# Performance work log

Measured on AMD Instinct MI355X. Metric: run time of the kernel, lower is better.

## Reference

```python
import jax, jax.numpy as jnp
import numpy as np

DIM = 128
GRID = 8
RED = 16  # LCBAM channel-attention reduction
B, L = 16, 4096


def setup_inputs() -> dict:
    key = jax.random.key(0)
    ks = jax.random.split(key, 8)
    scale = 1.0 / (np.sqrt(DIM) * np.sqrt(GRID))
    return {
        "x": jax.random.normal(ks[0], (B, L, DIM), jnp.float32),
        "n1_g": jnp.ones((DIM,), jnp.float32),
        "n1_b": jnp.zeros((DIM,), jnp.float32),
        "fk1_c": jax.random.normal(ks[1], (2, DIM, DIM, GRID), jnp.float32) * scale,
        "fk1_b": jnp.zeros((DIM,), jnp.float32),
        "n2_g": jnp.ones((DIM,), jnp.float32),
        "n2_b": jnp.zeros((DIM,), jnp.float32),
        "fk2_c": jax.random.normal(ks[2], (2, DIM, DIM, GRID), jnp.float32) * scale,
        "fk2_b": jnp.zeros((DIM,), jnp.float32),
        "w1": jax.random.normal(ks[3], (DIM // RED, DIM), jnp.float32) * 0.05,  # channel-MLP reduce
        "w2": jax.random.normal(ks[4], (DIM, DIM // RED), jnp.float32) * 0.05,  # channel-MLP expand
        "conv_w": jax.random.normal(ks[5], (1, 2, 7, 7), jnp.float32) * 0.05,   # spatial-attn 7x7 conv
    }


def _layernorm(x, g, b, eps=1e-5):
    m = jnp.mean(x, axis=-1, keepdims=True)
    v = jnp.var(x, axis=-1, keepdims=True)
    return (x - m) * jax.lax.rsqrt(v + eps) * g + b


def _fkan(x, coeffs, bias):
    # x: (B,L,I); coeffs: (2,O,I,G)
    k = jnp.arange(1, GRID + 1, dtype=x.dtype)          # (G,)
    ang = x[..., None] * k                               # (B,L,I,G)
    y = jnp.einsum("blig,oig->blo", jnp.cos(ang), coeffs[0])
    y = y + jnp.einsum("blig,oig->blo", jnp.sin(ang), coeffs[1])
    return y + bias


def reference(x, n1_g, n1_b, fk1_c, fk1_b, n2_g, n2_b, fk2_c, fk2_b, w1, w2, conv_w):
    residual = x
    out = _fkan(_layernorm(x, n1_g, n1_b), fk1_c, fk1_b)
    out = jax.nn.relu(out)
    out = _fkan(_layernorm(out, n2_g, n2_b), fk2_c, fk2_b)
    b, l, c = out.shape
    x4 = out.reshape(b, c, 1, l)  # faithful to torch .view (raw reshape, not transpose)
    # LCBAM channel attention: avg+max pool -> shared MLP -> sigmoid
    avg = jnp.mean(x4, axis=(2, 3))   # (B,C)
    mx = jnp.max(x4, axis=(2, 3))     # (B,C)
    mlp = lambda v: jax.nn.relu(v @ w1.T) @ w2.T
    ca = jax.nn.sigmoid(mlp(avg) + mlp(mx))[:, :, None, None]
    x4 = x4 * ca
    # LCBAM spatial attention: channel mean/max -> 7x7 conv -> sigmoid
    s_in = jnp.concatenate([jnp.mean(x4, axis=1, keepdims=True),
                            jnp.max(x4, axis=1, keepdims=True)], axis=1)  # (B,2,1,L)
    sa = jax.lax.conv_general_dilated(s_in, conv_w, (1, 1), ((3, 3), (3, 3)))
    x4 = x4 * jax.nn.sigmoid(sa)
    out = x4.reshape(b, l, c)
    return residual + out
```

## Files before the change

kernel.cpp:

```cpp
#include <hip/hip_runtime.h>
#include <math.h>

typedef unsigned short ushort_t;
typedef unsigned int uint_t;
typedef _Float16 half_t;

#define DIMC 128
#define NB 16
#define NL 4096

using f32x4 = __attribute__((ext_vector_type(4))) float;
using bf16x8 = __attribute__((ext_vector_type(8))) short;
using half4 = __attribute__((ext_vector_type(4))) half_t;

__device__ __forceinline__ ushort_t bf16rne(float f) {
  uint_t b = __float_as_uint(f);
  b += 0x7fffu + ((b >> 16) & 1u);
  return (ushort_t)(b >> 16);
}

__device__ __forceinline__ uint_t pkbf(float lo, float hi) {
  union { __bf16 h[2]; uint_t u; } u;
  u.h[0] = (__bf16)lo;
  u.h[1] = (__bf16)hi;
  return u.u;
}

__device__ __forceinline__ float bf2f(ushort_t u) {
  return __uint_as_float(((uint_t)u) << 16);
}

__global__ __launch_bounds__(256) void prep_coef_k(const float* __restrict__ fk1,
                                                   const float* __restrict__ fk2,
                                                   ushort_t* __restrict__ coefT) {
  int idx = blockIdx.x * 256 + threadIdx.x;
  int layer = idx >> 15;
  int rem = idx & 32767;
  int ci = rem >> 11;
  int n = (rem >> 8) & 7;
  int s = (rem >> 6) & 3;
  int l = rem & 63;
  int o = n * 16 + (l & 15);
  int kbase = ci * 128 + s * 32 + (l >> 4) * 8;
  const float* src = layer ? fk2 : fk1;
  uint_t p[4];
#pragma unroll
  for (int jj = 0; jj < 4; ++jj) {
    int k0 = kbase + jj * 2;
    int t0 = k0 & 1, g0 = (k0 >> 1) & 7, i0 = k0 >> 4;
    int k1 = k0 + 1;
    int t1 = k1 & 1, g1 = (k1 >> 1) & 7, i1 = k1 >> 4;
    ushort_t a = bf16rne(src[((t0 * DIMC + o) * DIMC + i0) * 8 + g0]);
    ushort_t b = bf16rne(src[((t1 * DIMC + o) * DIMC + i1) * 8 + g1]);
    p[jj] = (uint_t)a | ((uint_t)b << 16);
  }
  uint4 w;
  w.x = p[0]; w.y = p[1]; w.z = p[2]; w.w = p[3];
  *(uint4*)&coefT[idx * 8] = w;
}

constexpr int SXH = 132;

__global__ __launch_bounds__(256, 3) void fkan_main_k(
    const float* __restrict__ x,
    const float* __restrict__ n1g, const float* __restrict__ n1b,
    const float* __restrict__ fk1b,
    const float* __restrict__ n2g, const float* __restrict__ n2b,
    const float* __restrict__ fk2b,
    const ushort_t* __restrict__ coefT,
    ushort_t* __restrict__ out2,
    float* __restrict__ chanSum, float* __restrict__ chanMax) {

  __shared__ half_t xln[128 * SXH];

  const int tid = threadIdx.x;
  const int bid = blockIdx.x;
  const int lane = tid & 63;
  const int wid = tid >> 6;
  const int rowBase = wid * 32;
  const size_t tileBase = (size_t)bid * 128 * DIMC;

  {
    const float4* src = (const float4*)(x + tileBase + (size_t)rowBase * DIMC);
#pragma unroll
    for (int j = 0; j < 16; ++j) {
      int idx = j * 64 + lane;
      float4 v = src[idx];
      half4 h;
      h.x = (half_t)v.x; h.y = (half_t)v.y; h.z = (half_t)v.z; h.w = (half_t)v.w;
      *(half4*)&xln[(rowBase + (idx >> 5)) * SXH + (idx & 31) * 4] = h;
    }
  }

  auto layernorm = [&](const float* gg, const float* bb) {
    float g0 = gg[lane], g1 = gg[lane + 64];
    float be0 = bb[lane], be1 = bb[lane + 64];
#pragma unroll
    for (int j = 0; j < 32; ++j) {
      int t = rowBase + j;
      float v0 = (float)xln[t * SXH + lane], v1 = (float)xln[t * SXH + 64 + lane];
      float s = v0 + v1, q = v0 * v0 + v1 * v1;
#pragma unroll
      for (int m = 1; m < 64; m <<= 1) {
        s += __shfl_xor(s, m, 64);
        q += __shfl_xor(q, m, 64);
      }
      float mean = s * (1.0f / DIMC);
      float var = q * (1.0f / DIMC) - mean * mean;
      float rr = rsqrtf(var + 1e-5f);
      xln[t * SXH + lane] = (half_t)((v0 - mean) * rr * g0 + be0);
      xln[t * SXH + 64 + lane] = (half_t)((v1 - mean) * rr * g1 + be1);
    }
  };

  layernorm(n1g, n1b);

  const int hi = lane >> 4;
  const int hb = hi & 1;
  const half_t* xfr = &xln[(rowBase + (lane & 15)) * SXH + (hi >> 1)];

  auto featfrag = [&](int ci, int s, int mm) -> bf16x8 {
    float a = (float)xfr[mm * 16 * SXH + ci * 8 + s * 2];
    float s1, c1, s5, c5;
    __sincosf(a, &s1, &c1);
    __sincosf(5.0f * a, &s5, &c5);
    float cs = hb ? c5 : c1;
    float ss = hb ? s5 : s1;
    uint_t p0 = pkbf(cs, ss);
    float cn, sn;
    cn = cs * c1 - ss * s1; sn = ss * c1 + cs * s1; cs = cn; ss = sn;
    uint_t p1 = pkbf(cs, ss);
    cn = cs * c1 - ss * s1; sn = ss * c1 + cs * s1; cs = cn; ss = sn;
    uint_t p2 = pkbf(cs, ss);
    cn = cs * c1 - ss * s1; sn = ss * c1 + cs * s1; cs = cn; ss = sn;
    uint_t p3 = pkbf(cs, ss);
    union { uint_t u[4]; bf16x8 v; } r;
    r.u[0] = p0; r.u[1] = p1; r.u[2] = p2; r.u[3] = p3;
    return r.v;
  };

  f32x4 acc[8][2];

  auto ldB = [&](const ushort_t* cbase, int ci, int s, bf16x8 (&bf)[8]) {
#pragma unroll
    for (int nn = 0; nn < 8; ++nn)
      bf[nn] = *(const bf16x8*)(cbase +
          (size_t)((((ci * 8 + nn) * 4 + s) << 6) + lane) * 8);
  };

  auto mfma16 = [&](bf16x8 a0, bf16x8 a1, bf16x8 (&bf)[8]) {
    __builtin_amdgcn_s_setprio(1);
#pragma unroll
    for (int nn = 0; nn < 8; ++nn) {
      acc[nn][0] = __builtin_amdgcn_mfma_f32_16x16x32_bf16(a0, bf[nn],
                                                           acc[nn][0], 0, 0, 0);
      acc[nn][1] = __builtin_amdgcn_mfma_f32_16x16x32_bf16(a1, bf[nn],
                                                           acc[nn][1], 0, 0, 0);
    }
    __builtin_amdgcn_s_setprio(0);
  };

  auto run_layer = [&](const ushort_t* cbase) {
#pragma unroll
    for (int nn = 0; nn < 8; ++nn)
#pragma unroll
      for (int mm = 0; mm < 2; ++mm) acc[nn][mm] = (f32x4)(0.f);
#pragma unroll 1
    for (int ci = 0; ci < 16; ++ci) {
#pragma unroll
      for (int s = 0; s < 4; ++s) {
        bf16x8 bf[8];
        ldB(cbase, ci, s, bf);
        bf16x8 a0 = featfrag(ci, s, 0);
        bf16x8 a1 = featfrag(ci, s, 1);
        mfma16(a0, a1, bf);
      }
    }
  };

  run_layer(coefT);

#pragma unroll
  for (int nn = 0; nn < 8; ++nn) {
    int o = nn * 16 + (lane & 15);
    float bia = fk1b[o];
#pragma unroll
    for (int mm = 0; mm < 2; ++mm) {
      int trow = rowBase + mm * 16 + (lane >> 4) * 4;
#pragma unroll
      for (int r = 0; r < 4; ++r)
        xln[(trow + r) * SXH + o] = (half_t)fmaxf(acc[nn][mm][r] + bia, 0.f);
    }
  }

  layernorm(n2g, n2b);

  run_layer(coefT + 262144);

  float ls = 0.f, lm = -INFINITY;
#pragma unroll
  for (int nn = 0; nn < 8; ++nn) {
    int o = nn * 16 + (lane & 15);
    float bia = fk2b[o];
#pragma unroll
    for (int mm = 0; mm < 2; ++mm) {
      int trow = rowBase + mm * 16 + (lane >> 4) * 4;
#pragma unroll
      for (int r = 0; r < 4; ++r) {
        float v = acc[nn][mm][r] + bia;
        out2[tileBase + (size_t)(trow + r) * DIMC + o] = bf16rne(v);
        ls += v;
        lm = fmaxf(lm, v);
      }
    }
  }
#pragma unroll
  for (int m = 1; m < 64; m <<= 1) {
    ls += __shfl_xor(ls, m, 64);
    lm = fmaxf(lm, __shfl_xor(lm, m, 64));
  }
  if (lane == 0) {
    chanSum[bid * 4 + wid] = ls;
    chanMax[bid * 4 + wid] = lm;
  }
}

__global__ __launch_bounds__(128) void tail_k(
    const float* __restrict__ x, const ushort_t* __restrict__ out2,
    const float* __restrict__ chanSum, const float* __restrict__ chanMax,
    const float* __restrict__ w1, const float* __restrict__ w2,
    const float* __restrict__ convw, float* __restrict__ dout) {
  int b = blockIdx.x >> 5;
  int t = blockIdx.x & 31;
  int c = threadIdx.x;
  __shared__ float avs[DIMC], mxs[DIMC], hh[16], cas[DIMC];
  __shared__ float sM[134], sX[134];

  avs[c] = chanSum[b * DIMC + c] * (1.0f / NL);
  mxs[c] = chanMax[b * DIMC + c];
  __syncthreads();
  if (c < 16) {
    const float* v = (c < 8) ? avs : mxs;
    float a = 0.f;
    for (int i = 0; i < DIMC; ++i) a += v[i] * w1[(c & 7) * DIMC + i];
    hh[c] = fmaxf(a, 0.f);
  }
  __syncthreads();
  {
    float z = 0.f;
#pragma unroll
    for (int r = 0; r < 8; ++r) z += (hh[r] + hh[8 + r]) * w2[c * 8 + r];
    cas[c] = 1.0f / (1.0f + expf(-z));
  }
  __syncthreads();

  const ushort_t* o2b = out2 + (size_t)b * NL * DIMC;
  float s = 0.f, m = -INFINITY;
#pragma unroll 4
  for (int c4 = 0; c4 < 128; ++c4) {
    float v = bf2f(o2b[(size_t)(c4 * 32 + t) * DIMC + c]) * cas[c4];
    s += v;
    m = fmaxf(m, v);
  }
  sM[c + 3] = s * (1.0f / DIMC);
  sX[c + 3] = m;
  if (c < 6) {
    bool left = c < 3;
    int tp = left ? t - 1 : t + 1;
    int cc = left ? 125 + c : c - 3;
    int di = left ? c : 131 + (c - 3);
    float ss = 0.f, mm2 = -INFINITY;
    if (tp >= 0 && tp < 32) {
#pragma unroll 4
      for (int c4 = 0; c4 < 128; ++c4) {
        float v = bf2f(o2b[(size_t)(c4 * 32 + tp) * DIMC + cc]) * cas[c4];
        ss += v;
        mm2 = fmaxf(mm2, v);
      }
      sM[di] = ss * (1.0f / DIMC);
      sX[di] = mm2;
    } else {
      sM[di] = 0.f;
      sX[di] = 0.f;
    }
  }
  __syncthreads();

  float sa = 0.f;
#pragma unroll
  for (int d = 0; d < 7; ++d)
    sa += convw[21 + d] * sM[c + d] + convw[70 + d] * sX[c + d];
  float sig = 1.0f / (1.0f + expf(-sa));

  const float* xb = x + (size_t)b * NL * DIMC;
  float* db = dout + (size_t)b * NL * DIMC;
#pragma unroll 2
  for (int c4 = 0; c4 < 128; ++c4) {
    size_t idx = (size_t)(c4 * 32 + t) * DIMC + c;
    db[idx] = xb[idx] + bf2f(o2b[idx]) * cas[c4] * sig;
  }
}

extern "C" void kernel_launch(void* const* d_in, const int* in_sizes, int n_in,
                              void* d_out, int out_size, void* d_ws, size_t ws_size,
                              hipStream_t stream) {
  const float* x = (const float*)d_in[0];
  const float* n1g = (const float*)d_in[1];
  const float* n1b = (const float*)d_in[2];
  const float* fk1c = (const float*)d_in[3];
  const float* fk1b = (const float*)d_in[4];
  const float* n2g = (const float*)d_in[5];
  const float* n2b = (const float*)d_in[6];
  const float* fk2c = (const float*)d_in[7];
  const float* fk2b = (const float*)d_in[8];
  const float* w1 = (const float*)d_in[9];
  const float* w2 = (const float*)d_in[10];
  const float* convw = (const float*)d_in[11];

  ushort_t* out2 = (ushort_t*)d_ws;
  ushort_t* coefT = out2 + 8388608;
  float* chanSum = (float*)(coefT + 524288);
  float* chanMax = chanSum + 2048;
  float* dout = (float*)d_out;

  prep_coef_k<<<256, 256, 0, stream>>>(fk1c, fk2c, coefT);
  fkan_main_k<<<512, 256, 0, stream>>>(x, n1g, n1b, fk1b, n2g, n2b,
                                       fk2b, coefT, out2, chanSum, chanMax);
  tail_k<<<NB * 32, 128, 0, stream>>>(x, out2, chanSum, chanMax, w1, w2, convw, dout);
}
```

Baseline: 153.3 us.

## Split FKAN K-reduction across wave pairs with smaller 64-row tiles

Each block now handles 64 rows instead of 128. The two waves of each pair split the input-channel (K) loop in half, then sum their partial accumulators through a new LDS exchange buffer before the bias/ReLU and output epilogues. The grid doubles to 1024 blocks, aiming to expose more waves per CU and shorten each wave's serial MFMA and sincos chain. In exchange it adds several block-wide barriers and an extra LDS round trip of accumulators. Total LDS per block also grows, which may limit how many blocks fit on a CU.

New measurement: 192.0 us. 25.2% more time.

```diff
diff --git a/kernel.cpp b/kernel.cpp
--- a/kernel.cpp
+++ b/kernel.cpp
@@ -71,33 +71,37 @@
     ushort_t* __restrict__ out2,
     float* __restrict__ chanSum, float* __restrict__ chanMax) {
 
-  __shared__ half_t xln[128 * SXH];
+  __shared__ half_t xln[64 * SXH];
+  __shared__ f32x4 xch[2][16][64];
 
   const int tid = threadIdx.x;
   const int bid = blockIdx.x;
   const int lane = tid & 63;
   const int wid = tid >> 6;
-  const int rowBase = wid * 32;
-  const size_t tileBase = (size_t)bid * 128 * DIMC;
+  const int tg = wid >> 1;
+  const int kh = wid & 1;
+  const int rowBase = tg * 32;
+  const size_t tileBase = (size_t)bid * 64 * DIMC;
 
   {
-    const float4* src = (const float4*)(x + tileBase + (size_t)rowBase * DIMC);
-#pragma unroll
-    for (int j = 0; j < 16; ++j) {
-      int idx = j * 64 + lane;
+    const float4* src = (const float4*)(x + tileBase);
+#pragma unroll
+    for (int j = 0; j < 8; ++j) {
+      int idx = tid + j * 256;
       float4 v = src[idx];
       half4 h;
       h.x = (half_t)v.x; h.y = (half_t)v.y; h.z = (half_t)v.z; h.w = (half_t)v.w;
-      *(half4*)&xln[(rowBase + (idx >> 5)) * SXH + (idx & 31) * 4] = h;
-    }
-  }
+      *(half4*)&xln[((idx >> 5)) * SXH + (idx & 31) * 4] = h;
+    }
+  }
+  __syncthreads();
 
   auto layernorm = [&](const float* gg, const float* bb) {
     float g0 = gg[lane], g1 = gg[lane + 64];
     float be0 = bb[lane], be1 = bb[lane + 64];
 #pragma unroll
-    for (int j = 0; j < 32; ++j) {
-      int t = rowBase + j;
+    for (int j = 0; j < 16; ++j) {
+      int t = wid * 16 + j;
       float v0 = (float)xln[t * SXH + lane], v1 = (float)xln[t * SXH + 64 + lane];
       float s = v0 + v1, q = v0 * v0 + v1 * v1;
 #pragma unroll
@@ -114,6 +118,7 @@
   };
 
   layernorm(n1g, n1b);
+  __syncthreads();
 
   const int hi = lane >> 4;
   const int hb = hi & 1;
@@ -165,8 +170,9 @@
     for (int nn = 0; nn < 8; ++nn)
 #pragma unroll
       for (int mm = 0; mm < 2; ++mm) acc[nn][mm] = (f32x4)(0.f);
+    const int ci0 = kh * 8;
 #pragma unroll 1
-    for (int ci = 0; ci < 16; ++ci) {
+    for (int ci = ci0; ci < ci0 + 8; ++ci) {
 #pragma unroll
       for (int s = 0; s < 4; ++s) {
         bf16x8 bf[8];
@@ -179,49 +185,74 @@
   };
 
   run_layer(coefT);
-
-#pragma unroll
-  for (int nn = 0; nn < 8; ++nn) {
-    int o = nn * 16 + (lane & 15);
-    float bia = fk1b[o];
-#pragma unroll
-    for (int mm = 0; mm < 2; ++mm) {
-      int trow = rowBase + mm * 16 + (lane >> 4) * 4;
-#pragma unroll
-      for (int r = 0; r < 4; ++r)
-        xln[(trow + r) * SXH + o] = (half_t)fmaxf(acc[nn][mm][r] + bia, 0.f);
-    }
-  }
+  __syncthreads();
+
+  if (kh == 1) {
+#pragma unroll
+    for (int nn = 0; nn < 8; ++nn)
+#pragma unroll
+      for (int mm = 0; mm < 2; ++mm) xch[tg][nn * 2 + mm][lane] = acc[nn][mm];
+  }
+  __syncthreads();
+  if (kh == 0) {
+#pragma unroll
+    for (int nn = 0; nn < 8; ++nn) {
+      int o = nn * 16 + (lane & 15);
+      float bia = fk1b[o];
+#pragma unroll
+      for (int mm = 0; mm < 2; ++mm) {
+        f32x4 p = xch[tg][nn * 2 + mm][lane];
+        int trow = rowBase + mm * 16 + (lane >> 4) * 4;
+#pragma unroll
+        for (int r = 0; r < 4; ++r)
+          xln[(trow + r) * SXH + o] =
+              (half_t)fmaxf(acc[nn][mm][r] + p[r] + bia, 0.f);
+      }
+    }
+  }
+  __syncthreads();
 
   layernorm(n2g, n2b);
+  __syncthreads();
 
   run_layer(coefT + 262144);
-
-  float ls = 0.f, lm = -INFINITY;
-#pragma unroll
-  for (int nn = 0; nn < 8; ++nn) {
-    int o = nn * 16 + (lane & 15);
-    float bia = fk2b[o];
-#pragma unroll
-    for (int mm = 0; mm < 2; ++mm) {
-      int trow = rowBase + mm * 16 + (lane >> 4) * 4;
-#pragma unroll
-      for (int r = 0; r < 4; ++r) {
-        float v = acc[nn][mm][r] + bia;
-        out2[tileBase + (size_t)(trow + r) * DIMC + o] = bf16rne(v);
-        ls += v;
-        lm = fmaxf(lm, v);
-      }
-    }
-  }
-#pragma unroll
-  for (int m = 1; m < 64; m <<= 1) {
-    ls += __shfl_xor(ls, m, 64);
-    lm = fmaxf(lm, __shfl_xor(lm, m, 64));
-  }
-  if (lane == 0) {
-    chanSum[bid * 4 + wid] = ls;
-    chanMax[bid * 4 + wid] = lm;
+  __syncthreads();
+
+  if (kh == 1) {
+#pragma unroll
+    for (int nn = 0; nn < 8; ++nn)
+#pragma unroll
+      for (int mm = 0; mm < 2; ++mm) xch[tg][nn * 2 + mm][lane] = acc[nn][mm];
+  }
+  __syncthreads();
+  if (kh == 0) {
+    float ls = 0.f, lm = -INFINITY;
+#pragma unroll
+    for (int nn = 0; nn < 8; ++nn) {
+      int o = nn * 16 + (lane & 15);
+      float bia = fk2b[o];
+#pragma unroll
+      for (int mm = 0; mm < 2; ++mm) {
+        f32x4 p = xch[tg][nn * 2 + mm][lane];
+        int trow = rowBase + mm * 16 + (lane >> 4) * 4;
+#pragma unroll
+        for (int r = 0; r < 4; ++r) {
+          float v = acc[nn][mm][r] + p[r] + bia;
+          out2[tileBase + (size_t)(trow + r) * DIMC + o] = bf16rne(v);
+          ls += v;
+          lm = fmaxf(lm, v);
+        }
+      }
+    }
+#pragma unroll
+    for (int m = 1; m < 64; m <<= 1) {
+      ls += __shfl_xor(ls, m, 64);
+      lm = fmaxf(lm, __shfl_xor(lm, m, 64));
+    }
+    if (lane == 0) {
+      chanSum[bid * 2 + tg] = ls;
+      chanMax[bid * 2 + tg] = lm;
+    }
   }
 }
 
@@ -324,7 +355,7 @@
   float* dout = (float*)d_out;
 
   prep_coef_k<<<256, 256, 0, stream>>>(fk1c, fk2c, coefT);
-  fkan_main_k<<<512, 256, 0, stream>>>(x, n1g, n1b, fk1b, n2g, n2b,
-                                       fk2b, coefT, out2, chanSum, chanMax);
+  fkan_main_k<<<1024, 256, 0, stream>>>(x, n1g, n1b, fk1b, n2g, n2b,
+                                        fk2b, coefT, out2, chanSum, chanMax);
   tail_k<<<NB * 32, 128, 0, stream>>>(x, out2, chanSum, chanMax, w1, w2, convw, dout);
 }
```

## Generate Fourier features via full 8-step recurrence into double-buffered LDS

Applied to the files above, without the earlier changes.

Each lane now computes one sincos and an 8-step angle-addition recurrence for a single input, writing packed bf16 cos/sin features into a per-wave double-buffered LDS staging area. MFMA A-fragments are then read back from LDS instead of each lane computing two sincos calls and a 4-step recurrence. The intent is to halve transcendental work and overlap feature generation for the next step with the current MFMAs. In exchange it adds LDS traffic and a longer recurrence chain, and drops the occupancy hint from 3 to 2 blocks per CU. The cross-lane LDS handoff has no explicit barrier, so it relies on intra-wave ordering.

Result: no change. 153.1 us (-0.1%).

```diff
diff --git a/kernel.cpp b/kernel.cpp
--- a/kernel.cpp
+++ b/kernel.cpp
@@ -61,7 +61,7 @@
 
 constexpr int SXH = 132;
 
-__global__ __launch_bounds__(256, 3) void fkan_main_k(
+__global__ __launch_bounds__(256, 2) void fkan_main_k(
     const float* __restrict__ x,
     const float* __restrict__ n1g, const float* __restrict__ n1b,
     const float* __restrict__ fk1b,
@@ -72,6 +72,7 @@
     float* __restrict__ chanSum, float* __restrict__ chanMax) {
 
   __shared__ half_t xln[128 * SXH];
+  __shared__ uint4 feat[4][2][2][64];
 
   const int tid = threadIdx.x;
   const int bid = blockIdx.x;
@@ -115,28 +116,36 @@
 
   layernorm(n1g, n1b);
 
-  const int hi = lane >> 4;
-  const int hb = hi & 1;
-  const half_t* xfr = &xln[(rowBase + (lane & 15)) * SXH + (hi >> 1)];
-
-  auto featfrag = [&](int ci, int s, int mm) -> bf16x8 {
-    float a = (float)xfr[mm * 16 * SXH + ci * 8 + s * 2];
-    float s1, c1, s5, c5;
+  const int tl = lane & 31;
+  const int chOff = lane >> 5;
+  const int mmw = tl >> 4;
+  const int l0 = (tl & 15) + (chOff << 5);
+  const half_t* xch = &xln[(rowBase + tl) * SXH + chOff];
+
+  auto chain_gen = [&](int chunk, int ns, int nbuf) {
+    float a = (float)xch[chunk * 8 + ns * 2];
+    float s1, c1;
     __sincosf(a, &s1, &c1);
-    __sincosf(5.0f * a, &s5, &c5);
-    float cs = hb ? c5 : c1;
-    float ss = hb ? s5 : s1;
-    uint_t p0 = pkbf(cs, ss);
-    float cn, sn;
-    cn = cs * c1 - ss * s1; sn = ss * c1 + cs * s1; cs = cn; ss = sn;
-    uint_t p1 = pkbf(cs, ss);
-    cn = cs * c1 - ss * s1; sn = ss * c1 + cs * s1; cs = cn; ss = sn;
-    uint_t p2 = pkbf(cs, ss);
-    cn = cs * c1 - ss * s1; sn = ss * c1 + cs * s1; cs = cn; ss = sn;
-    uint_t p3 = pkbf(cs, ss);
-    union { uint_t u[4]; bf16x8 v; } r;
-    r.u[0] = p0; r.u[1] = p1; r.u[2] = p2; r.u[3] = p3;
-    return r.v;
+    uint_t q0 = pkbf(c1, s1);
+    float ck = c1, sk = s1, cn, sn;
+    cn = ck * c1 - sk * s1; sn = sk * c1 + ck * s1; ck = cn; sk = sn;
+    uint_t q1 = pkbf(ck, sk);
+    cn = ck * c1 - sk * s1; sn = sk * c1 + ck * s1; ck = cn; sk = sn;
+    uint_t q2 = pkbf(ck, sk);
+    cn = ck * c1 - sk * s1; sn = sk * c1 + ck * s1; ck = cn; sk = sn;
+    uint_t q3 = pkbf(ck, sk);
+    cn = ck * c1 - sk * s1; sn = sk * c1 + ck * s1; ck = cn; sk = sn;
+    uint_t q4 = pkbf(ck, sk);
+    cn = ck * c1 - sk * s1; sn = sk * c1 + ck * s1; ck = cn; sk = sn;
+    uint_t q5 = pkbf(ck, sk);
+    cn = ck * c1 - sk * s1; sn = sk * c1 + ck * s1; ck = cn; sk = sn;
+    uint_t q6 = pkbf(ck, sk);
+    cn = ck * c1 - sk * s1; sn = sk * c1 + ck * s1; ck = cn; sk = sn;
+    uint_t q7 = pkbf(ck, sk);
+    uint4 w0; w0.x = q0; w0.y = q1; w0.z = q2; w0.w = q3;
+    uint4 w1; w1.x = q4; w1.y = q5; w1.z = q6; w1.w = q7;
+    feat[wid][nbuf][mmw][l0] = w0;
+    feat[wid][nbuf][mmw][l0 + 16] = w1;
   };
 
   f32x4 acc[8][2];
@@ -165,14 +174,18 @@
     for (int nn = 0; nn < 8; ++nn)
 #pragma unroll
       for (int mm = 0; mm < 2; ++mm) acc[nn][mm] = (f32x4)(0.f);
+    chain_gen(0, 0, 0);
 #pragma unroll 1
     for (int ci = 0; ci < 16; ++ci) {
 #pragma unroll
-      for (int s = 0; s < 4; ++s) {
+      for (int j = 0; j < 4; ++j) {
         bf16x8 bf[8];
-        ldB(cbase, ci, s, bf);
-        bf16x8 a0 = featfrag(ci, s, 0);
-        bf16x8 a1 = featfrag(ci, s, 1);
+        ldB(cbase, ci, j, bf);
+        const int cb = j & 1;
+        bf16x8 a0 = *(const bf16x8*)&feat[wid][cb][0][lane];
+        bf16x8 a1 = *(const bf16x8*)&feat[wid][cb][1][lane];
+        const int nstep = ci * 4 + j + 1;
+        chain_gen((nstep >> 2) & 15, nstep & 3, nstep & 1);
         mfma16(a0, a1, bf);
       }
     }
```

## Split output channels across wave pairs with 64-row tiles and more blocks

Applied to the files above, without the earlier changes.

Halves the row tile per block to 64 and splits the 128 output channels between pairs of waves, doubling the grid and raising the occupancy hint. Adds block barriers around the shared LayerNorm buffer and an LDS reduction for the per-block channel sums and maxima. The aim is more parallelism and smaller register and LDS footprints. The cost is that each wave pair recomputes the same sin/cos features, and the new barriers add synchronisation.

Measured after the change: 186.1 us. 21.4% more time.

```diff
diff --git a/kernel.cpp b/kernel.cpp
--- a/kernel.cpp
+++ b/kernel.cpp
@@ -61,7 +61,7 @@
 
 constexpr int SXH = 132;
 
-__global__ __launch_bounds__(256, 3) void fkan_main_k(
+__global__ __launch_bounds__(256, 4) void fkan_main_k(
     const float* __restrict__ x,
     const float* __restrict__ n1g, const float* __restrict__ n1b,
     const float* __restrict__ fk1b,
@@ -71,33 +71,37 @@
     ushort_t* __restrict__ out2,
     float* __restrict__ chanSum, float* __restrict__ chanMax) {
 
-  __shared__ half_t xln[128 * SXH];
+  __shared__ half_t xln[64 * SXH];
+  __shared__ float sredS[2][2], sredM[2][2];
 
   const int tid = threadIdx.x;
   const int bid = blockIdx.x;
   const int lane = tid & 63;
   const int wid = tid >> 6;
-  const int rowBase = wid * 32;
-  const size_t tileBase = (size_t)bid * 128 * DIMC;
+  const int tg = wid >> 1;
+  const int nh = wid & 1;
+  const int rowBase = tg * 32;
+  const size_t tileBase = (size_t)bid * 64 * DIMC;
 
   {
-    const float4* src = (const float4*)(x + tileBase + (size_t)rowBase * DIMC);
-#pragma unroll
-    for (int j = 0; j < 16; ++j) {
-      int idx = j * 64 + lane;
+    const float4* src = (const float4*)(x + tileBase);
+#pragma unroll
+    for (int j = 0; j < 8; ++j) {
+      int idx = j * 256 + tid;
       float4 v = src[idx];
       half4 h;
       h.x = (half_t)v.x; h.y = (half_t)v.y; h.z = (half_t)v.z; h.w = (half_t)v.w;
-      *(half4*)&xln[(rowBase + (idx >> 5)) * SXH + (idx & 31) * 4] = h;
-    }
-  }
+      *(half4*)&xln[(idx >> 5) * SXH + (idx & 31) * 4] = h;
+    }
+  }
+  __syncthreads();
 
   auto layernorm = [&](const float* gg, const float* bb) {
     float g0 = gg[lane], g1 = gg[lane + 64];
     float be0 = bb[lane], be1 = bb[lane + 64];
 #pragma unroll
-    for (int j = 0; j < 32; ++j) {
-      int t = rowBase + j;
+    for (int j = 0; j < 16; ++j) {
+      int t = wid * 16 + j;
       float v0 = (float)xln[t * SXH + lane], v1 = (float)xln[t * SXH + 64 + lane];
       float s = v0 + v1, q = v0 * v0 + v1 * v1;
 #pragma unroll
@@ -114,6 +118,7 @@
   };
 
   layernorm(n1g, n1b);
+  __syncthreads();
 
   const int hi = lane >> 4;
   const int hb = hi & 1;
@@ -139,75 +144,78 @@
     return r.v;
   };
 
-  f32x4 acc[8][2];
-
-  auto ldB = [&](const ushort_t* cbase, int ci, int s, bf16x8 (&bf)[8]) {
-#pragma unroll
-    for (int nn = 0; nn < 8; ++nn)
-      bf[nn] = *(const bf16x8*)(cbase +
-          (size_t)((((ci * 8 + nn) * 4 + s) << 6) + lane) * 8);
-  };
-
-  auto mfma16 = [&](bf16x8 a0, bf16x8 a1, bf16x8 (&bf)[8]) {
+  f32x4 acc[4][2];
+
+  auto ldB = [&](const ushort_t* cbase, int ci, int s, bf16x8 (&bf)[4]) {
+#pragma unroll
+    for (int nt = 0; nt < 4; ++nt)
+      bf[nt] = *(const bf16x8*)(cbase +
+          (size_t)((((ci * 8 + nh * 4 + nt) * 4 + s) << 6) + lane) * 8);
+  };
+
+  auto mfma8 = [&](bf16x8 a0, bf16x8 a1, bf16x8 (&bf)[4]) {
     __builtin_amdgcn_s_setprio(1);
 #pragma unroll
-    for (int nn = 0; nn < 8; ++nn) {
-      acc[nn][0] = __builtin_amdgcn_mfma_f32_16x16x32_bf16(a0, bf[nn],
-                                                           acc[nn][0], 0, 0, 0);
-      acc[nn][1] = __builtin_amdgcn_mfma_f32_16x16x32_bf16(a1, bf[nn],
-                                                           acc[nn][1], 0, 0, 0);
+    for (int nt = 0; nt < 4; ++nt) {
+      acc[nt][0] = __builtin_amdgcn_mfma_f32_16x16x32_bf16(a0, bf[nt],
+                                                           acc[nt][0], 0, 0, 0);
+      acc[nt][1] = __builtin_amdgcn_mfma_f32_16x16x32_bf16(a1, bf[nt],
+                                                           acc[nt][1], 0, 0, 0);
     }
     __builtin_amdgcn_s_setprio(0);
   };
 
   auto run_layer = [&](const ushort_t* cbase) {
 #pragma unroll
-    for (int nn = 0; nn < 8; ++nn)
-#pragma unroll
-      for (int mm = 0; mm < 2; ++mm) acc[nn][mm] = (f32x4)(0.f);
+    for (int nt = 0; nt < 4; ++nt)
+#pragma unroll
+      for (int mm = 0; mm < 2; ++mm) acc[nt][mm] = (f32x4)(0.f);
 #pragma unroll 1
     for (int ci = 0; ci < 16; ++ci) {
 #pragma unroll
       for (int s = 0; s < 4; ++s) {
-        bf16x8 bf[8];
+        bf16x8 bf[4];
         ldB(cbase, ci, s, bf);
         bf16x8 a0 = featfrag(ci, s, 0);
         bf16x8 a1 = featfrag(ci, s, 1);
-        mfma16(a0, a1, bf);
+        mfma8(a0, a1, bf);
       }
     }
   };
 
   run_layer(coefT);
-
-#pragma unroll
-  for (int nn = 0; nn < 8; ++nn) {
-    int o = nn * 16 + (lane & 15);
+  __syncthreads();
+
+#pragma unroll
+  for (int nt = 0; nt < 4; ++nt) {
+    int o = (nh * 4 + nt) * 16 + (lane & 15);
     float bia = fk1b[o];
 #pragma unroll
     for (int mm = 0; mm < 2; ++mm) {
       int trow = rowBase + mm * 16 + (lane >> 4) * 4;
 #pragma unroll
       for (int r = 0; r < 4; ++r)
-        xln[(trow + r) * SXH + o] = (half_t)fmaxf(acc[nn][mm][r] + bia, 0.f);
-    }
-  }
+        xln[(trow + r) * SXH + o] = (half_t)fmaxf(acc[nt][mm][r] + bia, 0.f);
+    }
+  }
+  __syncthreads();
 
   layernorm(n2g, n2b);
+  __syncthreads();
 
   run_layer(coefT + 262144);
 
   float ls = 0.f, lm = -INFINITY;
 #pragma unroll
-  for (int nn = 0; nn < 8; ++nn) {
-    int o = nn * 16 + (lane & 15);
+  for (int nt = 0; nt < 4; ++nt) {
+    int o = (nh * 4 + nt) * 16 + (lane & 15);
     float bia = fk2b[o];
 #pragma unroll
     for (int mm = 0; mm < 2; ++mm) {
       int trow = rowBase + mm * 16 + (lane >> 4) * 4;
 #pragma unroll
       for (int r = 0; r < 4; ++r) {
-        float v = acc[nn][mm][r] + bia;
+        float v = acc[nt][mm][r] + bia;
         out2[tileBase + (size_t)(trow + r) * DIMC + o] = bf16rne(v);
         ls += v;
         lm = fmaxf(lm, v);
@@ -219,9 +227,11 @@
     ls += __shfl_xor(ls, m, 64);
     lm = fmaxf(lm, __shfl_xor(lm, m, 64));
   }
-  if (lane == 0) {
-    chanSum[bid * 4 + wid] = ls;
-    chanMax[bid * 4 + wid] = lm;
+  if (lane == 0) { sredS[tg][nh] = ls; sredM[tg][nh] = lm; }
+  __syncthreads();
+  if (tid < 2) {
+    chanSum[bid * 2 + tid] = sredS[tid][0] + sredS[tid][1];
+    chanMax[bid * 2 + tid] = fmaxf(sredM[tid][0], sredM[tid][1]);
   }
 }
 
@@ -324,7 +334,7 @@
   float* dout = (float*)d_out;
 
   prep_coef_k<<<256, 256, 0, stream>>>(fk1c, fk2c, coefT);
-  fkan_main_k<<<512, 256, 0, stream>>>(x, n1g, n1b, fk1b, n2g, n2b,
-                                       fk2b, coefT, out2, chanSum, chanMax);
+  fkan_main_k<<<1024, 256, 0, stream>>>(x, n1g, n1b, fk1b, n2g, n2b,
+                                        fk2b, coefT, out2, chanSum, chanMax);
   tail_k<<<NB * 32, 128, 0, stream>>>(x, out2, chanSum, chanMax, w1, w2, convw, dout);
 }
```
